# Performance work log

Measured on AMD Instinct MI355X. Metric: run time of the kernel, lower is better.

## Reference

```python
import jax, jax.numpy as jnp
import numpy as np

HID = 128


def setup_inputs() -> dict:
    key = jax.random.key(0)
    ks = jax.random.split(key, 7)
    B = 131072
    X = jax.random.normal(ks[0], (B, 4), dtype=jnp.float32)
    # Linear params stored as (in, out); scaled ~ 1/sqrt(fan_in) like torch default
    W1 = jax.random.normal(ks[1], (4, HID), dtype=jnp.float32) * 0.5
    b1 = jnp.zeros((HID,), jnp.float32)
    W2 = jax.random.normal(ks[2], (HID, HID), dtype=jnp.float32) * (1.0 / np.sqrt(HID))
    b2 = jnp.zeros((HID,), jnp.float32)
    W3 = jax.random.normal(ks[3], (HID, 1), dtype=jnp.float32) * (1.0 / np.sqrt(HID))
    b3 = jnp.zeros((1,), jnp.float32)
    return {"X": X, "W1": W1, "b1": b1, "W2": W2, "b2": b2, "W3": W3, "b3": b3}


def reference(X, W1, b1, W2, b2, W3, b3):
    def V_fn(feat):  # feat: [4] -> scalar potential
        h = jnp.tanh(feat @ W1 + b1)
        h = jnp.tanh(h @ W2 + b2)
        return (h @ W3 + b3)[0]

    def L_single(q, qd):  # q:[2], qd:[2] -> scalar Lagrangian
        t1, t2 = q[0], q[1]
        w1, w2 = qd[0], qd[1]
        T = w1 ** 2 + 0.5 * w2 ** 2 + w1 * w2 * jnp.cos(t1 - t2)
        feat = jnp.stack([jnp.sin(t1), jnp.cos(t1), jnp.sin(t2), jnp.cos(t2)])
        return T - V_fn(feat)

    q = X[:, :2]
    qd = X[:, 2:]
    dL_dq = jax.vmap(jax.grad(L_single, argnums=0))(q, qd)          # [B,2]
    # mass matrix M[i,j] = d^2 L / (d qd_i d qd_j)
    M = jax.vmap(jax.jacfwd(jax.grad(L_single, argnums=1), argnums=1))(q, qd)  # [B,2,2]
    # cross Hessian H[i,j] = d^2 L / (d qd_i d q_j); Coriolis C_i = H[i,:] @ qd
    H = jax.vmap(jax.jacfwd(jax.grad(L_single, argnums=1), argnums=0))(q, qd)  # [B,2,2]
    C = jnp.einsum('bij,bj->bi', H, qd)                              # [B,2]
    qdd = jnp.linalg.solve(M, (dL_dq - C)[..., None])[..., 0]        # [B,2]
    return jnp.concatenate([qd, qdd], axis=1)                        # [B,4]
```

## Files before the change

### kernel.cpp

```cpp
#include <hip/hip_runtime.h>
#include <math.h>

#define HID 128
#define TPB 1024
#define NW  16
#define GRIDB 256

typedef __bf16 bf16;
typedef bf16 bf16x8 __attribute__((ext_vector_type(8)));
typedef bf16 bf16x4 __attribute__((ext_vector_type(4)));
typedef float floatx4 __attribute__((ext_vector_type(4)));

__device__ __forceinline__ floatx4 tanh4(floatx4 z) {
    floatx4 t = z * 2.885390081777927f;
    floatx4 e = { __builtin_amdgcn_exp2f(t[0]), __builtin_amdgcn_exp2f(t[1]),
                  __builtin_amdgcn_exp2f(t[2]), __builtin_amdgcn_exp2f(t[3]) };
    e = e + 1.0f;
    floatx4 r = { __builtin_amdgcn_rcpf(e[0]), __builtin_amdgcn_rcpf(e[1]),
                  __builtin_amdgcn_rcpf(e[2]), __builtin_amdgcn_rcpf(e[3]) };
    return 1.0f - 2.0f * r;
}


__global__ __launch_bounds__(TPB, 4)
void lnn_kernel(const float* __restrict__ X,
                const float* __restrict__ W1,
                const float* __restrict__ b1,
                const float* __restrict__ b2,
                const float* __restrict__ W3,
                const float* __restrict__ W2,
                float* __restrict__ out,
                int B, int nchunk)
{
    __shared__ __align__(16) bf16 sW2A[16384];
    __shared__ __align__(16) bf16 sW2R[16384];
    __shared__ __align__(16) bf16 sH1w[NW][2048];
    __shared__ __align__(16) bf16 sGl[NW][512];
    __shared__ __align__(16) float sW1r[4][HID];
    __shared__ __align__(16) float sB1[HID], sB2[HID], sW3[HID];

    const int tid  = threadIdx.x;
    const int w    = tid >> 6;
    const int lane = tid & 63;
    const int lrow = lane & 15;
    const int lq   = lane >> 4;

    if (tid < 512) { int r = tid >> 7, j = tid & (HID - 1); sW1r[r][j] = W1[r * HID + j]; }
    if (tid < HID) sB1[tid] = b1[tid];
    else if (tid < 2 * HID) sB2[tid - HID] = b2[tid - HID];
    else if (tid < 3 * HID) sW3[tid - 2 * HID] = W3[tid - 2 * HID];

    #pragma unroll
    for (int tt = 0; tt < 2; ++tt) {
        int e = tid + tt * TPB;
        int t = e >> 6, l = e & 63;
        int a = t >> 2, bidx = t & 3;
        int lr = l & 15, q = l >> 4;
        bf16x8 f;
        #pragma unroll
        for (int idx = 0; idx < 8; ++idx)
            f[idx] = (bf16)W2[(32*bidx + 8*q + idx) * HID + 16*a + lr];
        *reinterpret_cast<bf16x8*>(&sW2A[e * 8]) = f;
        const float4* rp = reinterpret_cast<const float4*>(&W2[(16*a + lr) * HID + 32*bidx + 8*q]);
        float4 r0 = rp[0], r1 = rp[1];
        bf16x8 g;
        g[0]=(bf16)r0.x; g[1]=(bf16)r0.y; g[2]=(bf16)r0.z; g[3]=(bf16)r0.w;
        g[4]=(bf16)r1.x; g[5]=(bf16)r1.y; g[6]=(bf16)r1.z; g[7]=(bf16)r1.w;
        *reinterpret_cast<bf16x8*>(&sW2R[e * 8]) = g;
    }
    bf16x8 bW1[4];
    #pragma unroll
    for (int m = 0; m < 4; ++m) { bf16x8 z = {}; bW1[m] = z; }
    if (lrow < 4) {
        #pragma unroll
        for (int m = 0; m < 4; ++m) {
            const float4* wp = reinterpret_cast<const float4*>(&W1[lrow*HID + 32*m + 8*lq]);
            float4 a = wp[0], b = wp[1];
            bW1[m][0]=(bf16)a.x; bW1[m][1]=(bf16)a.y; bW1[m][2]=(bf16)a.z; bW1[m][3]=(bf16)a.w;
            bW1[m][4]=(bf16)b.x; bW1[m][5]=(bf16)b.y; bW1[m][6]=(bf16)b.z; bW1[m][7]=(bf16)b.w;
        }
    }
    __syncthreads();

    bf16* const myH = &sH1w[w][0];
    bf16* const myG = &sGl[w][0];

    const int tileStride = GRIDB * NW;
    const int t0 = (int)blockIdx.x * NW + w;
    int gc0 = t0 * 16 + lrow; gc0 = gc0 < B ? gc0 : (B - 1);
    float4 xc = reinterpret_cast<const float4*>(X)[gc0];

    #pragma unroll 1
    for (int c = 0; c < nchunk; ++c) {
        const int tile = t0 + c * tileStride;
        if (tile * 16 >= B) break;
        const int S0 = tile * 16;

        float s1, c1, s2, c2;
        __sincosf(xc.x, &s1, &c1);
        __sincosf(xc.y, &s2, &c2);
        const float qd1 = xc.z, qd2 = xc.w;

        float4 xn = xc;
        {
            int tn = tile + tileStride;
            if (tn * 16 < B) {
                int gc = tn * 16 + lrow; gc = gc < B ? gc : (B - 1);
                xn = reinterpret_cast<const float4*>(X)[gc];
            }
        }

        bf16x8 breg[4];
        #pragma unroll
        for (int kt = 0; kt < 4; ++kt) {
            int jb = 32 * kt + 8 * lq;
            floatx4 w0a = *reinterpret_cast<const floatx4*>(&sW1r[0][jb]);
            floatx4 w0b = *reinterpret_cast<const floatx4*>(&sW1r[0][jb+4]);
            floatx4 w1a = *reinterpret_cast<const floatx4*>(&sW1r[1][jb]);
            floatx4 w1b = *reinterpret_cast<const floatx4*>(&sW1r[1][jb+4]);
            floatx4 w2a = *reinterpret_cast<const floatx4*>(&sW1r[2][jb]);
            floatx4 w2b = *reinterpret_cast<const floatx4*>(&sW1r[2][jb+4]);
            floatx4 w3a = *reinterpret_cast<const floatx4*>(&sW1r[3][jb]);
            floatx4 w3b = *reinterpret_cast<const floatx4*>(&sW1r[3][jb+4]);
            floatx4 bba = *reinterpret_cast<const floatx4*>(&sB1[jb]);
            floatx4 bbb = *reinterpret_cast<const floatx4*>(&sB1[jb+4]);
            floatx4 za = bba + s1*w0a + c1*w1a + s2*w2a + c2*w3a;
            floatx4 zb = bbb + s1*w0b + c1*w1b + s2*w2b + c2*w3b;
            floatx4 ha = tanh4(za);
            floatx4 hb = tanh4(zb);
            bf16x8 hf;
            hf[0]=(bf16)ha[0]; hf[1]=(bf16)ha[1]; hf[2]=(bf16)ha[2]; hf[3]=(bf16)ha[3];
            hf[4]=(bf16)hb[0]; hf[5]=(bf16)hb[1]; hf[6]=(bf16)hb[2]; hf[7]=(bf16)hb[3];
            breg[kt] = hf;
            *reinterpret_cast<bf16x8*>(&myH[(kt*64 + lane)*8]) = hf;
        }

        floatx4 acc[8];
        #pragma unroll
        for (int jt = 0; jt < 8; ++jt) acc[jt] = floatx4{0.f,0.f,0.f,0.f};
        #pragma unroll
        for (int jt = 0; jt < 8; ++jt)
            #pragma unroll
            for (int kt = 0; kt < 4; ++kt)
                acc[jt] = __builtin_amdgcn_mfma_f32_16x16x32_bf16(
                    *reinterpret_cast<const bf16x8*>(&sW2A[((jt*4 + kt)*64 + lane)*8]),
                    breg[kt], acc[jt], 0,0,0);

        floatx4 acc2[8];
        #pragma unroll
        for (int it = 0; it < 8; ++it) acc2[it] = floatx4{0.f,0.f,0.f,0.f};
        #pragma unroll
        for (int jt2 = 0; jt2 < 4; ++jt2) {
            #pragma unroll
            for (int b = 0; b < 2; ++b) {
                int jt = 2*jt2 + b;
                int jb = 16*jt + 4*lq;
                floatx4 b2v = *reinterpret_cast<const floatx4*>(&sB2[jb]);
                floatx4 w3v = *reinterpret_cast<const floatx4*>(&sW3[jb]);
                floatx4 h = tanh4(acc[jt] + b2v);
                floatx4 gv = (1.0f - h*h) * w3v;
                bf16x4 g;
                g[0]=(bf16)gv[0]; g[1]=(bf16)gv[1]; g[2]=(bf16)gv[2]; g[3]=(bf16)gv[3];
                *reinterpret_cast<bf16x4*>(&myG[((2*b + (lq>>1))*16 + lrow)*8 + 4*(lq&1)]) = g;
            }
            bf16x8 gB = *reinterpret_cast<const bf16x8*>(&myG[lane*8]);
            #pragma unroll
            for (int it = 0; it < 8; ++it)
                acc2[it] = __builtin_amdgcn_mfma_f32_16x16x32_bf16(
                    *reinterpret_cast<const bf16x8*>(&sW2R[((it*4 + jt2)*64 + lane)*8]),
                    gB, acc2[it], 0,0,0);
        }

        #pragma unroll
        for (int it = 0; it < 8; ++it) {
            int off = ((it>>1)*64 + ((2*(it&1) + (lq>>1))*16 + lrow))*8 + 4*(lq&1);
            bf16x4 h4 = *reinterpret_cast<const bf16x4*>(&myH[off]);
            floatx4 hf = { (float)h4[0], (float)h4[1], (float)h4[2], (float)h4[3] };
            floatx4 gv = (1.0f - hf*hf) * acc2[it];
            bf16x4 g;
            g[0]=(bf16)gv[0]; g[1]=(bf16)gv[1]; g[2]=(bf16)gv[2]; g[3]=(bf16)gv[3];
            *reinterpret_cast<bf16x4*>(&myH[off]) = g;
        }

        floatx4 dv = floatx4{0.f,0.f,0.f,0.f};
        #pragma unroll
        for (int m = 0; m < 4; ++m)
            dv = __builtin_amdgcn_mfma_f32_16x16x32_bf16(
                bW1[m],
                *reinterpret_cast<const bf16x8*>(&myH[(m*64 + lane)*8]),
                dv, 0,0,0);

        if (lane < 16 && S0 + lane < B) {
            float dV0 = dv[0], dV1 = dv[1], dV2 = dv[2], dV3 = dv[3];
            float cosD = c1 * c2 + s1 * s2;
            float sinD = s1 * c2 - c1 * s2;
            float dVt1 = dV0 * c1 - dV1 * s1;
            float dVt2 = dV2 * c2 - dV3 * s2;
            float sT = qd1 * qd2 * sinD;
            float cw = sinD * (qd2 - qd1);
            float rhs1 = (-sT - dVt1) - qd2 * cw;
            float rhs2 = ( sT - dVt2) - qd1 * cw;
            float det = 2.0f - cosD * cosD;
            float inv = __builtin_amdgcn_rcpf(det);
            float qdd1 = (rhs1 - cosD * rhs2) * inv;
            float qdd2 = (2.0f * rhs2 - cosD * rhs1) * inv;
            *reinterpret_cast<float4*>(&out[4 * (S0 + lane)]) = make_float4(qd1, qd2, qdd1, qdd2);
        }
        xc = xn;
    }
}

extern "C" void kernel_launch(void* const* d_in, const int* in_sizes, int n_in,
                              void* d_out, int out_size, void* d_ws, size_t ws_size,
                              hipStream_t stream) {
    const float* X  = (const float*)d_in[0];
    const float* W1 = (const float*)d_in[1];
    const float* b1 = (const float*)d_in[2];
    const float* W2 = (const float*)d_in[3];
    const float* b2 = (const float*)d_in[4];
    const float* W3 = (const float*)d_in[5];
    float* out = (float*)d_out;
    int B = in_sizes[0] / 4;
    int tiles = (B + 15) >> 4;
    int nchunk = (tiles + GRIDB * NW - 1) / (GRIDB * NW);
    lnn_kernel<<<GRIDB, TPB, 0, stream>>>(X, W1, b1, b2, W3, W2, out, B, nchunk);
}
```

Baseline: 88.61 us.

## Software-pipeline layer-1 of next tile and swizzle per-warp LDS scratch

```diff
diff --git a/kernel.cpp b/kernel.cpp
--- a/kernel.cpp
+++ b/kernel.cpp
@@ -34,8 +34,8 @@
 {
     __shared__ __align__(16) bf16 sW2A[16384];
     __shared__ __align__(16) bf16 sW2R[16384];
-    __shared__ __align__(16) bf16 sH1w[NW][2048];
-    __shared__ __align__(16) bf16 sGl[NW][512];
+    __shared__ __align__(16) bf16 sXf[NW][2048];
+    __shared__ __align__(16) bf16 sW1A[4][512];
     __shared__ __align__(16) float sW1r[4][HID];
     __shared__ __align__(16) float sB1[HID], sB2[HID], sW3[HID];
 
@@ -44,6 +44,7 @@
     const int lane = tid & 63;
     const int lrow = lane & 15;
     const int lq   = lane >> 4;
+    const int swz  = lrow & 3;
 
     if (tid < 512) { int r = tid >> 7, j = tid & (HID - 1); sW1r[r][j] = W1[r * HID + j]; }
     if (tid < HID) sB1[tid] = b1[tid];
@@ -68,49 +69,22 @@
         g[4]=(bf16)r1.x; g[5]=(bf16)r1.y; g[6]=(bf16)r1.z; g[7]=(bf16)r1.w;
         *reinterpret_cast<bf16x8*>(&sW2R[e * 8]) = g;
     }
-    bf16x8 bW1[4];
-    #pragma unroll
-    for (int m = 0; m < 4; ++m) { bf16x8 z = {}; bW1[m] = z; }
-    if (lrow < 4) {
-        #pragma unroll
-        for (int m = 0; m < 4; ++m) {
-            const float4* wp = reinterpret_cast<const float4*>(&W1[lrow*HID + 32*m + 8*lq]);
-            float4 a = wp[0], b = wp[1];
-            bW1[m][0]=(bf16)a.x; bW1[m][1]=(bf16)a.y; bW1[m][2]=(bf16)a.z; bW1[m][3]=(bf16)a.w;
-            bW1[m][4]=(bf16)b.x; bW1[m][5]=(bf16)b.y; bW1[m][6]=(bf16)b.z; bW1[m][7]=(bf16)b.w;
-        }
+    if (tid < 256) {
+        int m = tid >> 6, l = tid & 63;
+        int lr = l & 15, q = l >> 4;
+        bf16x8 f = {};
+        if (lr < 4) {
+            #pragma unroll
+            for (int idx = 0; idx < 8; ++idx)
+                f[idx] = (bf16)W1[lr * HID + 32*m + 8*q + idx];
+        }
+        *reinterpret_cast<bf16x8*>(&sW1A[m][l * 8]) = f;
     }
     __syncthreads();
 
-    bf16* const myH = &sH1w[w][0];
-    bf16* const myG = &sGl[w][0];
-
-    const int tileStride = GRIDB * NW;
-    const int t0 = (int)blockIdx.x * NW + w;
-    int gc0 = t0 * 16 + lrow; gc0 = gc0 < B ? gc0 : (B - 1);
-    float4 xc = reinterpret_cast<const float4*>(X)[gc0];
-
-    #pragma unroll 1
-    for (int c = 0; c < nchunk; ++c) {
-        const int tile = t0 + c * tileStride;
-        if (tile * 16 >= B) break;
-        const int S0 = tile * 16;
-
-        float s1, c1, s2, c2;
-        __sincosf(xc.x, &s1, &c1);
-        __sincosf(xc.y, &s2, &c2);
-        const float qd1 = xc.z, qd2 = xc.w;
-
-        float4 xn = xc;
-        {
-            int tn = tile + tileStride;
-            if (tn * 16 < B) {
-                int gc = tn * 16 + lrow; gc = gc < B ? gc : (B - 1);
-                xn = reinterpret_cast<const float4*>(X)[gc];
-            }
-        }
-
-        bf16x8 breg[4];
+    bf16* const myX = &sXf[w][0];
+
+    auto P1 = [&](float f0, float f1, float f2, float f3, bf16x8* dst) {
         #pragma unroll
         for (int kt = 0; kt < 4; ++kt) {
             int jb = 32 * kt + 8 * lq;
@@ -124,78 +98,118 @@
             floatx4 w3b = *reinterpret_cast<const floatx4*>(&sW1r[3][jb+4]);
             floatx4 bba = *reinterpret_cast<const floatx4*>(&sB1[jb]);
             floatx4 bbb = *reinterpret_cast<const floatx4*>(&sB1[jb+4]);
-            floatx4 za = bba + s1*w0a + c1*w1a + s2*w2a + c2*w3a;
-            floatx4 zb = bbb + s1*w0b + c1*w1b + s2*w2b + c2*w3b;
+            floatx4 za = bba + f0*w0a + f1*w1a + f2*w2a + f3*w3a;
+            floatx4 zb = bbb + f0*w0b + f1*w1b + f2*w2b + f3*w3b;
             floatx4 ha = tanh4(za);
             floatx4 hb = tanh4(zb);
             bf16x8 hf;
             hf[0]=(bf16)ha[0]; hf[1]=(bf16)ha[1]; hf[2]=(bf16)ha[2]; hf[3]=(bf16)ha[3];
             hf[4]=(bf16)hb[0]; hf[5]=(bf16)hb[1]; hf[6]=(bf16)hb[2]; hf[7]=(bf16)hb[3];
-            breg[kt] = hf;
-            *reinterpret_cast<bf16x8*>(&myH[(kt*64 + lane)*8]) = hf;
-        }
+            dst[kt] = hf;
+        }
+    };
+    auto loadX = [&](int t) -> float4 {
+        int gc = t * 16 + lrow; gc = gc < B ? gc : (B - 1);
+        return reinterpret_cast<const float4*>(X)[gc];
+    };
+
+    const int tileStride = GRIDB * NW;
+    const int t0 = (int)blockIdx.x * NW + w;
+    const floatx4 fz = floatx4{0.f,0.f,0.f,0.f};
+
+    float4 xc = loadX(t0);
+    float s1c, c1c, s2c, c2c;
+    __sincosf(xc.x, &s1c, &c1c);
+    __sincosf(xc.y, &s2c, &c2c);
+    float qd1 = xc.z, qd2 = xc.w;
+    bf16x8 bregc[4];
+    P1(s1c, c1c, s2c, c2c, bregc);
+
+    #pragma unroll 1
+    for (int c = 0; c < nchunk; ++c) {
+        const int tile = t0 + c * tileStride;
+        if (tile * 16 >= B) break;
+        const int S0 = tile * 16;
+        float4 xn = loadX(tile + tileStride);
 
         floatx4 acc[8];
         #pragma unroll
-        for (int jt = 0; jt < 8; ++jt) acc[jt] = floatx4{0.f,0.f,0.f,0.f};
-        #pragma unroll
-        for (int jt = 0; jt < 8; ++jt)
-            #pragma unroll
-            for (int kt = 0; kt < 4; ++kt)
+        for (int jt = 0; jt < 8; ++jt) {
+            acc[jt] = __builtin_amdgcn_mfma_f32_16x16x32_bf16(
+                *reinterpret_cast<const bf16x8*>(&sW2A[((jt*4 + 0)*64 + lane)*8]),
+                bregc[0], fz, 0,0,0);
+            #pragma unroll
+            for (int kt = 1; kt < 4; ++kt)
                 acc[jt] = __builtin_amdgcn_mfma_f32_16x16x32_bf16(
                     *reinterpret_cast<const bf16x8*>(&sW2A[((jt*4 + kt)*64 + lane)*8]),
-                    breg[kt], acc[jt], 0,0,0);
-
+                    bregc[kt], acc[jt], 0,0,0);
+        }
+
+        #pragma unroll
+        for (int jt = 0; jt < 8; ++jt) {
+            int jb = 16*jt + 4*lq;
+            floatx4 b2v = *reinterpret_cast<const floatx4*>(&sB2[jb]);
+            floatx4 w3v = *reinterpret_cast<const floatx4*>(&sW3[jb]);
+            floatx4 h = tanh4(acc[jt] + b2v);
+            floatx4 gv = (1.0f - h*h) * w3v;
+            bf16x4 g;
+            g[0]=(bf16)gv[0]; g[1]=(bf16)gv[1]; g[2]=(bf16)gv[2]; g[3]=(bf16)gv[3];
+            int blk = (2*(jt&1) + (lq>>1)) ^ swz;
+            *reinterpret_cast<bf16x4*>(&myX[(jt>>1)*512 + lrow*32 + blk*8 + 4*(lq&1)]) = g;
+        }
+        bf16x8 gB[4];
+        #pragma unroll
+        for (int L = 0; L < 4; ++L)
+            gB[L] = *reinterpret_cast<const bf16x8*>(&myX[L*512 + lrow*32 + (L==L ? ((lq ^ swz)*8) : 0)]);
         floatx4 acc2[8];
         #pragma unroll
-        for (int it = 0; it < 8; ++it) acc2[it] = floatx4{0.f,0.f,0.f,0.f};
-        #pragma unroll
-        for (int jt2 = 0; jt2 < 4; ++jt2) {
-            #pragma unroll
-            for (int b = 0; b < 2; ++b) {
-                int jt = 2*jt2 + b;
-                int jb = 16*jt + 4*lq;
-                floatx4 b2v = *reinterpret_cast<const floatx4*>(&sB2[jb]);
-                floatx4 w3v = *reinterpret_cast<const floatx4*>(&sW3[jb]);
-                floatx4 h = tanh4(acc[jt] + b2v);
-                floatx4 gv = (1.0f - h*h) * w3v;
-                bf16x4 g;
-                g[0]=(bf16)gv[0]; g[1]=(bf16)gv[1]; g[2]=(bf16)gv[2]; g[3]=(bf16)gv[3];
-                *reinterpret_cast<bf16x4*>(&myG[((2*b + (lq>>1))*16 + lrow)*8 + 4*(lq&1)]) = g;
-            }
-            bf16x8 gB = *reinterpret_cast<const bf16x8*>(&myG[lane*8]);
+        for (int it = 0; it < 8; ++it)
+            acc2[it] = __builtin_amdgcn_mfma_f32_16x16x32_bf16(
+                *reinterpret_cast<const bf16x8*>(&sW2R[((it*4 + 0)*64 + lane)*8]),
+                gB[0], fz, 0,0,0);
+        #pragma unroll
+        for (int jt2 = 1; jt2 < 4; ++jt2)
             #pragma unroll
             for (int it = 0; it < 8; ++it)
                 acc2[it] = __builtin_amdgcn_mfma_f32_16x16x32_bf16(
                     *reinterpret_cast<const bf16x8*>(&sW2R[((it*4 + jt2)*64 + lane)*8]),
-                    gB, acc2[it], 0,0,0);
-        }
+                    gB[jt2], acc2[it], 0,0,0);
+
+        float s1n, c1n, s2n, c2n;
+        __sincosf(xn.x, &s1n, &c1n);
+        __sincosf(xn.y, &s2n, &c2n);
+        bf16x8 bregn[4];
+        P1(s1n, c1n, s2n, c2n, bregn);
 
         #pragma unroll
         for (int it = 0; it < 8; ++it) {
-            int off = ((it>>1)*64 + ((2*(it&1) + (lq>>1))*16 + lrow))*8 + 4*(lq&1);
-            bf16x4 h4 = *reinterpret_cast<const bf16x4*>(&myH[off]);
-            floatx4 hf = { (float)h4[0], (float)h4[1], (float)h4[2], (float)h4[3] };
-            floatx4 gv = (1.0f - hf*hf) * acc2[it];
             bf16x4 g;
-            g[0]=(bf16)gv[0]; g[1]=(bf16)gv[1]; g[2]=(bf16)gv[2]; g[3]=(bf16)gv[3];
-            *reinterpret_cast<bf16x4*>(&myH[off]) = g;
-        }
-
-        floatx4 dv = floatx4{0.f,0.f,0.f,0.f};
-        #pragma unroll
-        for (int m = 0; m < 4; ++m)
+            g[0]=(bf16)acc2[it][0]; g[1]=(bf16)acc2[it][1];
+            g[2]=(bf16)acc2[it][2]; g[3]=(bf16)acc2[it][3];
+            int blk = (2*(it&1) + (lq>>1)) ^ swz;
+            *reinterpret_cast<bf16x4*>(&myX[(it>>1)*512 + lrow*32 + blk*8 + 4*(lq&1)]) = g;
+        }
+        floatx4 dv = fz;
+        #pragma unroll
+        for (int m = 0; m < 4; ++m) {
+            bf16x8 sv = *reinterpret_cast<const bf16x8*>(&myX[m*512 + lrow*32 + (lq ^ swz)*8]);
+            bf16x8 g1;
+            #pragma unroll
+            for (int idx = 0; idx < 8; ++idx) {
+                float h = (float)bregc[m][idx];
+                float s = (float)sv[idx];
+                g1[idx] = (bf16)(s - s*h*h);
+            }
             dv = __builtin_amdgcn_mfma_f32_16x16x32_bf16(
-                bW1[m],
-                *reinterpret_cast<const bf16x8*>(&myH[(m*64 + lane)*8]),
-                dv, 0,0,0);
+                *reinterpret_cast<const bf16x8*>(&sW1A[m][lane*8]), g1, dv, 0,0,0);
+        }
 
         if (lane < 16 && S0 + lane < B) {
             float dV0 = dv[0], dV1 = dv[1], dV2 = dv[2], dV3 = dv[3];
-            float cosD = c1 * c2 + s1 * s2;
-            float sinD = s1 * c2 - c1 * s2;
-            float dVt1 = dV0 * c1 - dV1 * s1;
-            float dVt2 = dV2 * c2 - dV3 * s2;
+            float cosD = c1c * c2c + s1c * s2c;
+            float sinD = s1c * c2c - c1c * s2c;
+            float dVt1 = dV0 * c1c - dV1 * s1c;
+            float dVt2 = dV2 * c2c - dV3 * s2c;
             float sT = qd1 * qd2 * sinD;
             float cw = sinD * (qd2 - qd1);
             float rhs1 = (-sT - dVt1) - qd2 * cw;
@@ -206,7 +220,9 @@
             float qdd2 = (2.0f * rhs2 - cosD * rhs1) * inv;
             *reinterpret_cast<float4*>(&out[4 * (S0 + lane)]) = make_float4(qd1, qd2, qdd1, qdd2);
         }
-        xc = xn;
+
+        bregc[0]=bregn[0]; bregc[1]=bregn[1]; bregc[2]=bregn[2]; bregc[3]=bregn[3];
+        s1c=s1n; c1c=c1n; s2c=s2n; c2c=c2n; qd1=xn.z; qd2=xn.w;
     }
 }
 
```

Result: slower. 121.8 us (+37.5%).
